# Performance work log

Hardware: AMD Instinct MI355X
Metric: run time of the kernel (lower is better)

Reference implementation:

```python
import jax, jax.numpy as jnp
import numpy as np

HIDDEN = 4096
N_HEADS = 32
N_KV = 8
HEAD_DIM = HIDDEN // N_HEADS  # 128
ROT_DIM = int(HEAD_DIM * 0.5)  # partial_rotary_factor = 0.5 -> 64
ROPE_BASE = 1_000_000.0
EPS = 1e-6
T = 2048


def setup_inputs() -> dict:
    key = jax.random.key(0)
    k1, k2, k3, k4, k5 = jax.random.split(key, 5)
    qkv_out = (N_HEADS + 2 * N_KV) * HEAD_DIM  # 6144
    hidden_states = jax.random.normal(k1, (T, HIDDEN), dtype=jnp.float32)
    positions = jnp.arange(T, dtype=jnp.int32)
    w_qkv = jax.random.normal(k2, (HIDDEN, qkv_out), dtype=jnp.float32) * (HIDDEN ** -0.5)
    w_o = jax.random.normal(k3, (N_HEADS * HEAD_DIM, HIDDEN), dtype=jnp.float32) * ((N_HEADS * HEAD_DIM) ** -0.5)
    q_norm_w = jnp.ones((HEAD_DIM,), dtype=jnp.float32) + 0.01 * jax.random.normal(k4, (HEAD_DIM,), dtype=jnp.float32)
    k_norm_w = jnp.ones((HEAD_DIM,), dtype=jnp.float32) + 0.01 * jax.random.normal(k5, (HEAD_DIM,), dtype=jnp.float32)
    return {"hidden_states": hidden_states, "positions": positions,
            "w_qkv": w_qkv, "w_o": w_o, "q_norm_w": q_norm_w, "k_norm_w": k_norm_w}


def _rms_norm(x, w):
    # x: [T, H, D]; normalize over last dim
    var = jnp.mean(jnp.square(x), axis=-1, keepdims=True)
    return x * jax.lax.rsqrt(var + EPS) * w


def _apply_rope(x, positions):
    # neox-style rotary on first ROT_DIM dims of head_dim; rest passes through
    half = ROT_DIM // 2
    inv_freq = 1.0 / (ROPE_BASE ** (jnp.arange(0, ROT_DIM, 2, dtype=jnp.float32) / ROT_DIM))
    freqs = positions.astype(jnp.float32)[:, None] * inv_freq[None, :]  # [T, half]
    cos = jnp.cos(freqs)[:, None, :]  # [T, 1, half]
    sin = jnp.sin(freqs)[:, None, :]
    x_rot, x_pass = x[..., :ROT_DIM], x[..., ROT_DIM:]
    x1, x2 = x_rot[..., :half], x_rot[..., half:]
    rot = jnp.concatenate([x1 * cos - x2 * sin, x2 * cos + x1 * sin], axis=-1)
    return jnp.concatenate([rot, x_pass], axis=-1)


def reference(hidden_states, positions, w_qkv, w_o, q_norm_w, k_norm_w):
    q_size = N_HEADS * HEAD_DIM
    kv_size = N_KV * HEAD_DIM
    qkv = hidden_states @ w_qkv  # [T, q+2kv]
    q = qkv[:, :q_size].reshape(-1, N_HEADS, HEAD_DIM)
    k = qkv[:, q_size:q_size + kv_size].reshape(-1, N_KV, HEAD_DIM)
    v = qkv[:, q_size + kv_size:].reshape(-1, N_KV, HEAD_DIM)
    q = _rms_norm(q, q_norm_w)
    k = _rms_norm(k, k_norm_w)
    q = _apply_rope(q, positions)
    k = _apply_rope(k, positions)
    # GQA: repeat kv heads
    rep = N_HEADS // N_KV
    k = jnp.repeat(k, rep, axis=1)  # [T, H, D]
    v = jnp.repeat(v, rep, axis=1)
    scale = HEAD_DIM ** -0.5
    scores = jnp.einsum('thd,shd->hts', q, k) * scale  # [H, T, T]
    t = hidden_states.shape[0]
    causal = jnp.tril(jnp.ones((t, t), dtype=bool))
    scores = jnp.where(causal[None], scores, jnp.float32(-1e30))
    probs = jax.nn.softmax(scores, axis=-1)
    o = jnp.einsum('hts,shd->thd', probs, v).reshape(t, N_HEADS * HEAD_DIM)
    return o @ w_o
```

## Files before the change

kernel.cpp:

```cpp
#include <hip/hip_runtime.h>
#include <math.h>

#define HIDDEN 4096
#define QKV_N 6144
#define T_LEN 2048
#define HD 128
#define N_HEADS 32
#define N_KV 8
#define SCALE 0.08838834764831845f

typedef unsigned short u16;
typedef unsigned int u32;
typedef __attribute__((ext_vector_type(8))) short bf16x8;
typedef __attribute__((ext_vector_type(4))) float f32x4;

__device__ __forceinline__ u16 f2b(float x) {
  u32 u = __builtin_bit_cast(u32, x);
  u += 0x7fffu + ((u >> 16) & 1u);
  return (u16)(u >> 16);
}

typedef const __attribute__((address_space(1))) void* gas_ptr;
typedef __attribute__((address_space(3))) void* las_ptr;
__device__ __forceinline__ void gll16(const void* g, void* l) {
  __builtin_amdgcn_global_load_lds((gas_ptr)g, (las_ptr)l, 16, 0, 0);
}

__global__ __launch_bounds__(256) void cast_bf16_kernel(
    const float* __restrict__ in, u16* __restrict__ out) {
  const size_t i = ((size_t)blockIdx.x * 256 + threadIdx.x) * 4;
  f32x4 v = *(const f32x4*)(in + i);
  ushort4 o;
  o.x = f2b(v[0]); o.y = f2b(v[1]); o.z = f2b(v[2]); o.w = f2b(v[3]);
  *(ushort4*)(out + i) = o;
}

__global__ __launch_bounds__(256) void transpose_cast_kernel(
    const float* __restrict__ W, u16* __restrict__ WT, int K, int N) {
  __shared__ float t[32][33];
  const int n0 = blockIdx.x * 32, k0 = blockIdx.y * 32;
  const int c = threadIdx.x & 31;
  const int r0 = threadIdx.x >> 5;
#pragma unroll
  for (int j = 0; j < 4; ++j) {
    const int r = r0 + 8 * j;
    t[c][r] = W[(size_t)(k0 + r) * N + n0 + c];
  }
  __syncthreads();
#pragma unroll
  for (int j = 0; j < 4; ++j) {
    const int n = r0 + 8 * j;
    WT[(size_t)(n0 + n) * K + k0 + c] = f2b(t[n][c]);
  }
}

template <int BM, int BN>
__global__ __launch_bounds__(512, 2) void gemm256_kernel(
    const u16* __restrict__ A, const u16* __restrict__ BT,
    float* __restrict__ C, int M, int N, int K) {
  constexpr int WCOLS = BN / 4;
  constexpr int NF = WCOLS / 16;
  constexpr int NF2 = NF / 2;
  constexpr int MF = BM / 32;
  constexpr int ALOADS = BM / 128;
  constexpr int BLOADS = BN / 128;
  constexpr int VMN = ALOADS + BLOADS;
  __shared__ __align__(16) u16 As[2][2][BM * 32];
  __shared__ __align__(16) u16 Bs[2][2][BN * 32];

  const int tid = threadIdx.x;
  const int w = tid >> 6, l = tid & 63;
  const int wr = w >> 2, wc = w & 3;
  const int m = l & 15, g = l >> 4;
  const int bm = blockIdx.y * BM, bn = blockIdx.x * BN;
  const int NT = K >> 6;

  size_t gA[2]; int sA[2];
  size_t gB[2]; int sB[2];
#pragma unroll
  for (int i = 0; i < ALOADS; ++i) {
    const int s = i * 512 + tid;
    const int r = s >> 2, o = s & 3;
    sA[i] = s * 8;
    gA[i] = (size_t)(bm + r) * K + (o ^ ((r >> 1) & 3)) * 8;
  }
#pragma unroll
  for (int i = 0; i < BLOADS; ++i) {
    const int s = i * 512 + tid;
    const int r = s >> 2, o = s & 3;
    sB[i] = s * 8;
    gB[i] = (size_t)(bn + r) * K + (o ^ ((r >> 1) & 3)) * 8;
  }

  const int foff = m * 32 + ((g ^ ((m >> 1) & 3)) * 8);
  const int abase = wr * (BM / 2) * 32;
  const int bbase = wc * WCOLS * 32;

#define STAGE_A(tile, kh)                                                      \
  {                                                                            \
    const size_t kofs = (size_t)(tile) * 64 + (kh) * 32;                       \
    u16* dst = &As[(tile) & 1][kh][0];                                         \
    gll16(A + gA[0] + kofs, dst + sA[0]);                                      \
    if constexpr (ALOADS > 1) gll16(A + gA[1] + kofs, dst + sA[1]);            \
  }
#define STAGE_B(tile, kh)                                                      \
  {                                                                            \
    const size_t kofs = (size_t)(tile) * 64 + (kh) * 32;                       \
    u16* dst = &Bs[(tile) & 1][kh][0];                                         \
    gll16(BT + gB[0] + kofs, dst + sB[0]);                                     \
    if constexpr (BLOADS > 1) gll16(BT + gB[1] + kofs, dst + sB[1]);           \
  }
#define VM_COUNTED()                                                           \
  {                                                                            \
    if constexpr (VMN == 4)                                                    \
      asm volatile("s_waitcnt vmcnt(4)" ::: "memory");                         \
    else                                                                       \
      asm volatile("s_waitcnt vmcnt(3)" ::: "memory");                         \
  }
#define PHASE(j, b, DO_STAGE, tn, VM)                                          \
  {                                                                            \
    constexpr int qn = (j) & 1, kh = (j) >> 1;                                 \
    if constexpr (qn == 0) {                                                   \
      _Pragma("unroll") for (int fm = 0; fm < MF; ++fm)                        \
          af[fm] = *(const bf16x8*)(&As[b][kh][abase + fm * 512 + foff]);      \
    }                                                                          \
    bf16x8 bf[NF2];                                                            \
    _Pragma("unroll") for (int fn = 0; fn < NF2; ++fn)                         \
        bf[fn] =                                                               \
        *(const bf16x8*)(&Bs[b][kh][bbase + (qn * NF2 + fn) * 512 + foff]);    \
    if constexpr (DO_STAGE) {                                                  \
      if constexpr ((j) == 0) STAGE_A(tn, 0);                                  \
      if constexpr ((j) == 1) STAGE_B(tn, 0);                                  \
      if constexpr ((j) == 2) STAGE_A(tn, 1);                                  \
      if constexpr ((j) == 3) STAGE_B(tn, 1);                                  \
    }                                                                          \
    asm volatile("" ::: "memory");                                             \
    __builtin_amdgcn_s_barrier();                                              \
    asm volatile("" ::: "memory");                                             \
    __builtin_amdgcn_s_setprio(1);                                             \
    _Pragma("unroll") for (int fm = 0; fm < MF; ++fm)                          \
        _Pragma("unroll") for (int fn = 0; fn < NF2; ++fn)                     \
        acc[fm][qn * NF2 + fn] = __builtin_amdgcn_mfma_f32_16x16x32_bf16(      \
            af[fm], bf[fn], acc[fm][qn * NF2 + fn], 0, 0, 0);                  \
    __builtin_amdgcn_s_setprio(0);                                             \
    asm volatile("" ::: "memory");                                             \
    if constexpr (((j) & 1) && (VM) == 0)                                      \
      asm volatile("s_waitcnt vmcnt(0)" ::: "memory");                         \
    if constexpr (((j) & 1) && (VM) == 1) VM_COUNTED();                        \
    __builtin_amdgcn_s_barrier();                                              \
    asm volatile("" ::: "memory");                                             \
  }

  f32x4 acc[MF][NF];
#pragma unroll
  for (int i = 0; i < MF; ++i)
#pragma unroll
    for (int j = 0; j < NF; ++j) acc[i][j] = (f32x4){0.f, 0.f, 0.f, 0.f};

  STAGE_A(0, 0); STAGE_B(0, 0); STAGE_A(0, 1); STAGE_B(0, 1);
  VM_COUNTED();
  __builtin_amdgcn_s_barrier();
  asm volatile("" ::: "memory");

  bf16x8 af[MF];
  for (int t = 0; t < NT - 1; ++t) {
    const int b = t & 1, tn = t + 1;
    PHASE(0, b, true, tn, 1);
    PHASE(1, b, true, tn, 1);
    PHASE(2, b, true, tn, 1);
    PHASE(3, b, true, tn, 1);
  }
  {
    const int b = (NT - 1) & 1;
    PHASE(0, b, false, 0, 2);
    PHASE(1, b, false, 0, 0);
    PHASE(2, b, false, 0, 2);
    PHASE(3, b, false, 0, 2);
  }
#undef PHASE
#undef VM_COUNTED
#undef STAGE_B
#undef STAGE_A

#pragma unroll
  for (int fm = 0; fm < MF; ++fm) {
    const int row = bm + wr * (BM / 2) + fm * 16 + g * 4;
#pragma unroll
    for (int fn = 0; fn < NF; ++fn) {
      const int col = bn + wc * WCOLS + fn * 16 + m;
      float* cp = C + (size_t)row * N + col;
#pragma unroll
      for (int r = 0; r < 4; ++r) cp[(size_t)r * N] = acc[fm][fn][r];
    }
  }
}

__global__ __launch_bounds__(128) void normrope_pack_kernel(
    const float* __restrict__ qkv, const int* __restrict__ positions,
    const float* __restrict__ qw, const float* __restrict__ kw,
    u16* __restrict__ Qp, u16* __restrict__ Kp) {
  const int t = blockIdx.x;
  const int hh = blockIdx.y;
  const int d = threadIdx.x;
  const bool isq = hh < N_HEADS;
  const int col = isq ? hh * HD : HIDDEN + (hh - N_HEADS) * HD;
  const float* row = qkv + (size_t)t * QKV_N + col;
  const float* w = isq ? qw : kw;

  float x = row[d];
  float ss = x * x;
#pragma unroll
  for (int off = 32; off >= 1; off >>= 1) ss += __shfl_xor(ss, off);
  __shared__ float wsum[2];
  __shared__ float xs[128];
  if ((d & 63) == 0) wsum[d >> 6] = ss;
  __syncthreads();
  const float tot = wsum[0] + wsum[1];
  const float inv = rsqrtf(tot * (1.f / 128.f) + 1e-6f);
  const float xn = x * inv * w[d];
  xs[d] = xn;
  __syncthreads();

  float outv;
  if (d < 64) {
    const int idx = d & 31;
    const float invf = powf(1.0e6f, -(float)idx * (1.0f / 32.0f));
    const float fr = (float)positions[t] * invf;
    const float c = cosf(fr), s = sinf(fr);
    const float x1 = xs[idx], x2 = xs[idx + 32];
    outv = (d < 32) ? (x1 * c - x2 * s) : (x2 * c + x1 * s);
  } else {
    outv = xn;
  }
  if (isq) {
    Qp[((size_t)hh * T_LEN + t) * HD + d] = f2b(outv * SCALE);
  } else {
    Kp[((size_t)(hh - N_HEADS) * T_LEN + t) * HD + d] = f2b(outv);
  }
}

__global__ __launch_bounds__(256) void vtrans_kernel(
    const float* __restrict__ qkv, u16* __restrict__ Vtp) {
  __shared__ float tile[32][132];
  const int t0 = blockIdx.x * 32;
  const int kvh = blockIdx.y;
  const int tv = threadIdx.x >> 3;
  const int c0 = (threadIdx.x & 7) * 16;
  const float* src =
      qkv + (size_t)(t0 + tv) * QKV_N + (HIDDEN + 1024) + kvh * HD + c0;
#pragma unroll
  for (int u = 0; u < 4; ++u)
    *(f32x4*)&tile[tv][c0 + 4 * u] = *(const f32x4*)(src + 4 * u);
  __syncthreads();
  const int dd = threadIdx.x >> 1;
  const int half = threadIdx.x & 1;
  u16 buf[16];
#pragma unroll
  for (int p = 0; p < 16; ++p) buf[p] = f2b(tile[half * 16 + p][dd]);
  u16* dst = Vtp + ((size_t)kvh * HD + dd) * T_LEN + t0 + half * 16;
  *(uint4*)dst = *(uint4*)&buf[0];
  *(uint4*)(dst + 8) = *(uint4*)&buf[8];
}

__global__ __launch_bounds__(256, 3) void attn4_kernel(
    const u16* __restrict__ Qp, const u16* __restrict__ Kp,
    const u16* __restrict__ Vtp, u16* __restrict__ outB) {
  __shared__ __align__(16) u16 Qs[64 * 128];
  __shared__ __align__(16) u16 Ks[2 * 32 * 128];
  __shared__ __align__(16) u16 Vts[2 * 128 * 32];
  __shared__ __align__(16) u16 Plds[4 * 16 * 32];

  const int bx = blockIdx.x;
  const int h = blockIdx.y;
  const int kvh = h >> 2;
  const int tid = threadIdx.x;
  const int w = tid >> 6, l = tid & 63;
  const int g = l >> 4, m = l & 15;

  const u16* kbase = Kp + (size_t)kvh * T_LEN * HD;
  const u16* vbase = Vtp + (size_t)kvh * HD * T_LEN;
  u16* pl = Plds + w * 512;

#define STAGE_KV(jt, b)                                                        \
  {                                                                            \
    _Pragma("unroll") for (int p = 0; p < 2; ++p) {                            \
      const int krow = p * 16 + w * 4 + (l >> 4);                              \
      const int kg = (l & 15) ^ (krow & 7);                                    \
      gll16(kbase + (size_t)((jt) * 32 + krow) * 128 + kg * 8,                 \
            Ks + (b) * 4096 + p * 2048 + w * 512 + l * 8);                     \
      const int dv = p * 64 + w * 16 + (l >> 2);                               \
      const int vg = (l & 3) ^ ((dv >> 1) & 3);                                \
      gll16(vbase + (size_t)dv * T_LEN + (jt) * 32 + vg * 8,                   \
            Vts + (b) * 4096 + p * 2048 + w * 512 + l * 8);                    \
    }                                                                          \
  }

  for (int job = 0; job < 2; ++job) {
    const int qb = job ? bx : 31 - bx;
    const int t0 = qb * 64;
    const int NT = 2 * (qb + 1);

    {
      const u16* qbase = Qp + ((size_t)h * T_LEN + t0) * HD;
#pragma unroll
      for (int p = 0; p < 4; ++p) {
        const int row = p * 16 + w * 4 + (l >> 4);
        const int gr = (l & 15) ^ (row & 7);
        gll16(qbase + row * 128 + gr * 8, Qs + p * 2048 + w * 512 + l * 8);
      }
    }
    STAGE_KV(0, 0);
    __syncthreads();

    bf16x8 qf[4];
    {
      const u16* qr = Qs + (w * 16 + m) * 128;
#pragma unroll
      for (int kk = 0; kk < 4; ++kk)
        qf[kk] = *(const bf16x8*)(qr + (((kk * 4 + g) ^ (m & 7)) * 8));
    }

    f32x4 o[8];
#pragma unroll
    for (int n = 0; n < 8; ++n) o[n] = (f32x4){0.f, 0.f, 0.f, 0.f};
    float mrun = -1e30f, lrun = 0.f;

    for (int jt = 0; jt < NT; ++jt) {
      const int b = jt & 1;
      if (jt + 1 < NT) STAGE_KV(jt + 1, b ^ 1);

      f32x4 s[2];
      s[0] = (f32x4){0.f, 0.f, 0.f, 0.f};
      s[1] = (f32x4){0.f, 0.f, 0.f, 0.f};
      __builtin_amdgcn_s_setprio(1);
#pragma unroll
      for (int f = 0; f < 2; ++f) {
        const u16* kr = Ks + b * 4096 + (f * 16 + m) * 128;
#pragma unroll
        for (int kk = 0; kk < 4; ++kk) {
          bf16x8 kf = *(const bf16x8*)(kr + (((kk * 4 + g) ^ (m & 7)) * 8));
          s[f] =
              __builtin_amdgcn_mfma_f32_16x16x32_bf16(kf, qf[kk], s[f], 0, 0, 0);
        }
      }
      __builtin_amdgcn_s_setprio(0);

      if (jt >= NT - 2) {
        const int qg = t0 + w * 16 + m;
        const int kvb = jt * 32 + g * 4;
#pragma unroll
        for (int f = 0; f < 2; ++f)
#pragma unroll
          for (int r = 0; r < 4; ++r)
            if (kvb + f * 16 + r > qg) s[f][r] = -1e30f;
      }

      float pm = fmaxf(fmaxf(fmaxf(s[0][0], s[0][1]), fmaxf(s[0][2], s[0][3])),
                       fmaxf(fmaxf(s[1][0], s[1][1]), fmaxf(s[1][2], s[1][3])));
      pm = fmaxf(pm, __shfl_xor(pm, 16));
      pm = fmaxf(pm, __shfl_xor(pm, 32));
      if (!__all(pm <= mrun + 8.f)) {
        const float mn = fmaxf(mrun, pm);
        const float sc = __expf(mrun - mn);
        mrun = mn;
        lrun *= sc;
        f32x4 scr;
#pragma unroll
        for (int r = 0; r < 4; ++r) scr[r] = __shfl(sc, g * 4 + r);
#pragma unroll
        for (int n = 0; n < 8; ++n) o[n] *= scr;
      }
      float ps = 0.f;
#pragma unroll
      for (int f = 0; f < 2; ++f)
#pragma unroll
        for (int r = 0; r < 4; ++r) {
          s[f][r] = __expf(s[f][r] - mrun);
          ps += s[f][r];
        }
      ps += __shfl_xor(ps, 16);
      ps += __shfl_xor(ps, 32);
      lrun += ps;

      {
        const u32 a0 = (u32)f2b(s[0][0]) | ((u32)f2b(s[0][1]) << 16);
        const u32 a1 = (u32)f2b(s[0][2]) | ((u32)f2b(s[0][3]) << 16);
        const u32 b0 = (u32)f2b(s[1][0]) | ((u32)f2b(s[1][1]) << 16);
        const u32 b1 = (u32)f2b(s[1][2]) | ((u32)f2b(s[1][3]) << 16);
        *(uint2*)(pl + m * 32 + ((g ^ (m >> 1)) * 4)) = make_uint2(a0, a1);
        *(uint2*)(pl + m * 32 + (((g + 4) ^ (m >> 1)) * 4)) = make_uint2(b0, b1);
      }

      bf16x8 pa;
      {
        const uint2 lo =
            *(const uint2*)(pl + m * 32 + (((2 * g) ^ (m >> 1)) * 4));
        const uint2 hi =
            *(const uint2*)(pl + m * 32 + (((2 * g + 1) ^ (m >> 1)) * 4));
        union { u32 u[4]; bf16x8 v; } pu;
        pu.u[0] = lo.x; pu.u[1] = lo.y; pu.u[2] = hi.x; pu.u[3] = hi.y;
        pa = pu.v;
      }

      __builtin_amdgcn_s_setprio(1);
#pragma unroll
      for (int n = 0; n < 8; ++n) {
        const int dd = n * 16 + m;
        bf16x8 vf = *(const bf16x8*)(Vts + b * 4096 + dd * 32 +
                                     ((g ^ ((dd >> 1) & 3)) * 8));
        o[n] = __builtin_amdgcn_mfma_f32_16x16x32_bf16(pa, vf, o[n], 0, 0, 0);
      }
      __builtin_amdgcn_s_setprio(0);
      __syncthreads();
    }

    float li[4];
#pragma unroll
    for (int r = 0; r < 4; ++r) li[r] = 1.f / __shfl(lrun, g * 4 + r);
    u16* ob = outB + (size_t)(t0 + w * 16 + g * 4) * HIDDEN + h * HD + m;
#pragma unroll
    for (int n = 0; n < 8; ++n)
#pragma unroll
      for (int r = 0; r < 4; ++r)
        ob[(size_t)r * HIDDEN + n * 16] = f2b(o[n][r] * li[r]);
  }
#undef STAGE_KV
}

extern "C" void kernel_launch(void* const* d_in, const int* in_sizes, int n_in,
                              void* d_out, int out_size, void* d_ws,
                              size_t ws_size, hipStream_t stream) {
  const float* hidden = (const float*)d_in[0];
  const int* positions = (const int*)d_in[1];
  const float* w_qkv = (const float*)d_in[2];
  const float* w_o = (const float*)d_in[3];
  const float* q_norm_w = (const float*)d_in[4];
  const float* k_norm_w = (const float*)d_in[5];
  float* out = (float*)d_out;

  u16* hiddenB = (u16*)d_ws;
  u16* Qp = hiddenB;
  u16* wqkvT = hiddenB + (size_t)T_LEN * HIDDEN;
  u16* woT = wqkvT + (size_t)QKV_N * HIDDEN;
  float* qkv = (float*)(woT + (size_t)HIDDEN * HIDDEN);
  u16* attnB = (u16*)(qkv + (size_t)T_LEN * QKV_N);
  u16* Kp = attnB + (size_t)T_LEN * HIDDEN;
  u16* Vtp = Kp + (size_t)N_KV * T_LEN * HD;

  cast_bf16_kernel<<<(T_LEN * HIDDEN) / 1024, 256, 0, stream>>>(hidden, hiddenB);
  transpose_cast_kernel<<<dim3(QKV_N / 32, HIDDEN / 32), 256, 0, stream>>>(
      w_qkv, wqkvT, HIDDEN, QKV_N);
  transpose_cast_kernel<<<dim3(HIDDEN / 32, HIDDEN / 32), 256, 0, stream>>>(
      w_o, woT, HIDDEN, HIDDEN);

  gemm256_kernel<256, 256><<<dim3(QKV_N / 256, T_LEN / 256), 512, 0, stream>>>(
      hiddenB, wqkvT, qkv, T_LEN, QKV_N, HIDDEN);
  normrope_pack_kernel<<<dim3(T_LEN, N_HEADS + N_KV), 128, 0, stream>>>(
      qkv, positions, q_norm_w, k_norm_w, Qp, Kp);
  vtrans_kernel<<<dim3(T_LEN / 32, N_KV), 256, 0, stream>>>(qkv, Vtp);
  attn4_kernel<<<dim3(16, N_HEADS), 256, 0, stream>>>(Qp, Kp, Vtp, attnB);
  gemm256_kernel<128, 256><<<dim3(HIDDEN / 256, T_LEN / 128), 512, 0, stream>>>(
      attnB, woT, out, T_LEN, HIDDEN, HIDDEN);
}
```

Baseline: 368.2 us.

## Double attention query tile per block to reuse K/V across two row groups

Each attention block now processes 128 query rows instead of 64, split into two 64-row halves per wave, so every staged K/V tile and its K fragments feed two sets of MFMAs. The causal early half skips work when a KV tile lies past its rows. This halves K/V global and LDS traffic per query row. In exchange, register pressure and LDS use rise, occupancy drops from 3 to 2 blocks per CU, and the grid shrinks to 256 blocks, which may underfill the GPU.

Result: slower. 394.1 us (+7.1%).

```diff
diff --git a/kernel.cpp b/kernel.cpp
--- a/kernel.cpp
+++ b/kernel.cpp
@@ -262,13 +262,13 @@
   *(uint4*)(dst + 8) = *(uint4*)&buf[8];
 }
 
-__global__ __launch_bounds__(256, 3) void attn4_kernel(
+__global__ __launch_bounds__(256, 2) void attn5_kernel(
     const u16* __restrict__ Qp, const u16* __restrict__ Kp,
     const u16* __restrict__ Vtp, u16* __restrict__ outB) {
-  __shared__ __align__(16) u16 Qs[64 * 128];
+  __shared__ __align__(16) u16 Qs[128 * 128];
   __shared__ __align__(16) u16 Ks[2 * 32 * 128];
   __shared__ __align__(16) u16 Vts[2 * 128 * 32];
-  __shared__ __align__(16) u16 Plds[4 * 16 * 32];
+  __shared__ __align__(16) u16 Plds[2 * 4 * 16 * 32];
 
   const int bx = blockIdx.x;
   const int h = blockIdx.y;
@@ -279,7 +279,8 @@
 
   const u16* kbase = Kp + (size_t)kvh * T_LEN * HD;
   const u16* vbase = Vtp + (size_t)kvh * HD * T_LEN;
-  u16* pl = Plds + w * 512;
+  u16* pl0 = Plds + w * 512;
+  u16* pl1 = Plds + 2048 + w * 512;
 
 #define STAGE_KV(jt, b)                                                        \
   {                                                                            \
@@ -294,16 +295,57 @@
             Vts + (b) * 4096 + p * 2048 + w * 512 + l * 8);                    \
     }                                                                          \
   }
+#define P_BOUNCE(sv, pl, pa)                                                   \
+  {                                                                            \
+    const u32 a0 = (u32)f2b(sv[0][0]) | ((u32)f2b(sv[0][1]) << 16);            \
+    const u32 a1 = (u32)f2b(sv[0][2]) | ((u32)f2b(sv[0][3]) << 16);            \
+    const u32 b0 = (u32)f2b(sv[1][0]) | ((u32)f2b(sv[1][1]) << 16);            \
+    const u32 b1 = (u32)f2b(sv[1][2]) | ((u32)f2b(sv[1][3]) << 16);            \
+    *(uint2*)((pl) + m * 32 + ((g ^ (m >> 1)) * 4)) = make_uint2(a0, a1);      \
+    *(uint2*)((pl) + m * 32 + (((g + 4) ^ (m >> 1)) * 4)) = make_uint2(b0, b1);\
+    const uint2 lo = *(const uint2*)((pl) + m * 32 + (((2 * g) ^ (m >> 1)) * 4)); \
+    const uint2 hi =                                                           \
+        *(const uint2*)((pl) + m * 32 + (((2 * g + 1) ^ (m >> 1)) * 4));       \
+    union { u32 u[4]; bf16x8 v; } pu;                                          \
+    pu.u[0] = lo.x; pu.u[1] = lo.y; pu.u[2] = hi.x; pu.u[3] = hi.y;            \
+    pa = pu.v;                                                                 \
+  }
+#define SOFTMAX_SET(sv, mrun, lrun, ov)                                        \
+  {                                                                            \
+    float pm = fmaxf(fmaxf(fmaxf(sv[0][0], sv[0][1]), fmaxf(sv[0][2], sv[0][3])), \
+                     fmaxf(fmaxf(sv[1][0], sv[1][1]), fmaxf(sv[1][2], sv[1][3]))); \
+    pm = fmaxf(pm, __shfl_xor(pm, 16));                                        \
+    pm = fmaxf(pm, __shfl_xor(pm, 32));                                        \
+    if (!__all(pm <= mrun + 8.f)) {                                            \
+      const float mn = fmaxf(mrun, pm);                                        \
+      const float sc = __expf(mrun - mn);                                      \
+      mrun = mn;                                                               \
+      lrun *= sc;                                                              \
+      f32x4 scr;                                                               \
+      _Pragma("unroll") for (int r = 0; r < 4; ++r) scr[r] =                   \
+          __shfl(sc, g * 4 + r);                                               \
+      _Pragma("unroll") for (int n = 0; n < 8; ++n) ov[n] *= scr;              \
+    }                                                                          \
+    float ps = 0.f;                                                            \
+    _Pragma("unroll") for (int f = 0; f < 2; ++f)                              \
+        _Pragma("unroll") for (int r = 0; r < 4; ++r) {                        \
+      sv[f][r] = __expf(sv[f][r] - mrun);                                      \
+      ps += sv[f][r];                                                          \
+    }                                                                          \
+    ps += __shfl_xor(ps, 16);                                                  \
+    ps += __shfl_xor(ps, 32);                                                  \
+    lrun += ps;                                                                \
+  }
 
   for (int job = 0; job < 2; ++job) {
-    const int qb = job ? bx : 31 - bx;
-    const int t0 = qb * 64;
-    const int NT = 2 * (qb + 1);
+    const int qb = job ? bx : 15 - bx;
+    const int t0 = qb * 128;
+    const int NT = 4 * (qb + 1);
 
     {
       const u16* qbase = Qp + ((size_t)h * T_LEN + t0) * HD;
 #pragma unroll
-      for (int p = 0; p < 4; ++p) {
+      for (int p = 0; p < 8; ++p) {
         const int row = p * 16 + w * 4 + (l >> 4);
         const int gr = (l & 15) ^ (row & 7);
         gll16(qbase + row * 128 + gr * 8, Qs + p * 2048 + w * 512 + l * 8);
@@ -312,94 +354,87 @@
     STAGE_KV(0, 0);
     __syncthreads();
 
-    bf16x8 qf[4];
+    bf16x8 qf0[4], qf1[4];
     {
-      const u16* qr = Qs + (w * 16 + m) * 128;
-#pragma unroll
-      for (int kk = 0; kk < 4; ++kk)
-        qf[kk] = *(const bf16x8*)(qr + (((kk * 4 + g) ^ (m & 7)) * 8));
+      const u16* qr0 = Qs + (w * 16 + m) * 128;
+      const u16* qr1 = Qs + (64 + w * 16 + m) * 128;
+#pragma unroll
+      for (int kk = 0; kk < 4; ++kk) {
+        const int go = ((kk * 4 + g) ^ (m & 7)) * 8;
+        qf0[kk] = *(const bf16x8*)(qr0 + go);
+        qf1[kk] = *(const bf16x8*)(qr1 + go);
+      }
     }
 
-    f32x4 o[8];
-#pragma unroll
-    for (int n = 0; n < 8; ++n) o[n] = (f32x4){0.f, 0.f, 0.f, 0.f};
-    float mrun = -1e30f, lrun = 0.f;
+    f32x4 o0[8], o1[8];
+#pragma unroll
+    for (int n = 0; n < 8; ++n) {
+      o0[n] = (f32x4){0.f, 0.f, 0.f, 0.f};
+      o1[n] = (f32x4){0.f, 0.f, 0.f, 0.f};
+    }
+    float mrun0 = -1e30f, lrun0 = 0.f, mrun1 = -1e30f, lrun1 = 0.f;
+    const int qg0 = t0 + w * 16 + m;
+    const int qg1 = t0 + 64 + w * 16 + m;
 
     for (int jt = 0; jt < NT; ++jt) {
       const int b = jt & 1;
       if (jt + 1 < NT) STAGE_KV(jt + 1, b ^ 1);
-
-      f32x4 s[2];
-      s[0] = (f32x4){0.f, 0.f, 0.f, 0.f};
-      s[1] = (f32x4){0.f, 0.f, 0.f, 0.f};
+      const bool do0 = (jt * 32 <= t0 + 63);
+
+      bf16x8 kfr[8];
+#pragma unroll
+      for (int f = 0; f < 2; ++f)
+#pragma unroll
+        for (int kk = 0; kk < 4; ++kk)
+          kfr[f * 4 + kk] = *(const bf16x8*)(
+              Ks + b * 4096 + (f * 16 + m) * 128 + (((kk * 4 + g) ^ (m & 7)) * 8));
+
+      f32x4 s1[2];
+      s1[0] = (f32x4){0.f, 0.f, 0.f, 0.f};
+      s1[1] = (f32x4){0.f, 0.f, 0.f, 0.f};
+      f32x4 s0[2];
       __builtin_amdgcn_s_setprio(1);
 #pragma unroll
-      for (int f = 0; f < 2; ++f) {
-        const u16* kr = Ks + b * 4096 + (f * 16 + m) * 128;
-#pragma unroll
-        for (int kk = 0; kk < 4; ++kk) {
-          bf16x8 kf = *(const bf16x8*)(kr + (((kk * 4 + g) ^ (m & 7)) * 8));
-          s[f] =
-              __builtin_amdgcn_mfma_f32_16x16x32_bf16(kf, qf[kk], s[f], 0, 0, 0);
-        }
+      for (int f = 0; f < 2; ++f)
+#pragma unroll
+        for (int kk = 0; kk < 4; ++kk)
+          s1[f] = __builtin_amdgcn_mfma_f32_16x16x32_bf16(kfr[f * 4 + kk],
+                                                          qf1[kk], s1[f], 0, 0, 0);
+      if (do0) {
+        s0[0] = (f32x4){0.f, 0.f, 0.f, 0.f};
+        s0[1] = (f32x4){0.f, 0.f, 0.f, 0.f};
+#pragma unroll
+        for (int f = 0; f < 2; ++f)
+#pragma unroll
+          for (int kk = 0; kk < 4; ++kk)
+            s0[f] = __builtin_amdgcn_mfma_f32_16x16x32_bf16(
+                kfr[f * 4 + kk], qf0[kk], s0[f], 0, 0, 0);
       }
       __builtin_amdgcn_s_setprio(0);
 
       if (jt >= NT - 2) {
-        const int qg = t0 + w * 16 + m;
         const int kvb = jt * 32 + g * 4;
 #pragma unroll
         for (int f = 0; f < 2; ++f)
 #pragma unroll
           for (int r = 0; r < 4; ++r)
-            if (kvb + f * 16 + r > qg) s[f][r] = -1e30f;
-      }
-
-      float pm = fmaxf(fmaxf(fmaxf(s[0][0], s[0][1]), fmaxf(s[0][2], s[0][3])),
-                       fmaxf(fmaxf(s[1][0], s[1][1]), fmaxf(s[1][2], s[1][3])));
-      pm = fmaxf(pm, __shfl_xor(pm, 16));
-      pm = fmaxf(pm, __shfl_xor(pm, 32));
-      if (!__all(pm <= mrun + 8.f)) {
-        const float mn = fmaxf(mrun, pm);
-        const float sc = __expf(mrun - mn);
-        mrun = mn;
-        lrun *= sc;
-        f32x4 scr;
-#pragma unroll
-        for (int r = 0; r < 4; ++r) scr[r] = __shfl(sc, g * 4 + r);
-#pragma unroll
-        for (int n = 0; n < 8; ++n) o[n] *= scr;
-      }
-      float ps = 0.f;
-#pragma unroll
-      for (int f = 0; f < 2; ++f)
-#pragma unroll
-        for (int r = 0; r < 4; ++r) {
-          s[f][r] = __expf(s[f][r] - mrun);
-          ps += s[f][r];
-        }
-      ps += __shfl_xor(ps, 16);
-      ps += __shfl_xor(ps, 32);
-      lrun += ps;
-
-      {
-        const u32 a0 = (u32)f2b(s[0][0]) | ((u32)f2b(s[0][1]) << 16);
-        const u32 a1 = (u32)f2b(s[0][2]) | ((u32)f2b(s[0][3]) << 16);
-        const u32 b0 = (u32)f2b(s[1][0]) | ((u32)f2b(s[1][1]) << 16);
-        const u32 b1 = (u32)f2b(s[1][2]) | ((u32)f2b(s[1][3]) << 16);
-        *(uint2*)(pl + m * 32 + ((g ^ (m >> 1)) * 4)) = make_uint2(a0, a1);
-        *(uint2*)(pl + m * 32 + (((g + 4) ^ (m >> 1)) * 4)) = make_uint2(b0, b1);
-      }
-
-      bf16x8 pa;
-      {
-        const uint2 lo =
-            *(const uint2*)(pl + m * 32 + (((2 * g) ^ (m >> 1)) * 4));
-        const uint2 hi =
-            *(const uint2*)(pl + m * 32 + (((2 * g + 1) ^ (m >> 1)) * 4));
-        union { u32 u[4]; bf16x8 v; } pu;
-        pu.u[0] = lo.x; pu.u[1] = lo.y; pu.u[2] = hi.x; pu.u[3] = hi.y;
-        pa = pu.v;
+            if (kvb + f * 16 + r > qg1) s1[f][r] = -1e30f;
+      }
+      if (do0 && jt >= NT - 4) {
+        const int kvb = jt * 32 + g * 4;
+#pragma unroll
+        for (int f = 0; f < 2; ++f)
+#pragma unroll
+          for (int r = 0; r < 4; ++r)
+            if (kvb + f * 16 + r > qg0) s0[f][r] = -1e30f;
+      }
+
+      bf16x8 pa0, pa1;
+      SOFTMAX_SET(s1, mrun1, lrun1, o1);
+      P_BOUNCE(s1, pl1, pa1);
+      if (do0) {
+        SOFTMAX_SET(s0, mrun0, lrun0, o0);
+        P_BOUNCE(s0, pl0, pa0);
       }
 
       __builtin_amdgcn_s_setprio(1);
@@ -408,22 +443,32 @@
         const int dd = n * 16 + m;
         bf16x8 vf = *(const bf16x8*)(Vts + b * 4096 + dd * 32 +
                                      ((g ^ ((dd >> 1) & 3)) * 8));
-        o[n] = __builtin_amdgcn_mfma_f32_16x16x32_bf16(pa, vf, o[n], 0, 0, 0);
+        o1[n] = __builtin_amdgcn_mfma_f32_16x16x32_bf16(pa1, vf, o1[n], 0, 0, 0);
+        if (do0)
+          o0[n] = __builtin_amdgcn_mfma_f32_16x16x32_bf16(pa0, vf, o0[n], 0, 0, 0);
       }
       __builtin_amdgcn_s_setprio(0);
       __syncthreads();
     }
 
-    float li[4];
-#pragma unroll
-    for (int r = 0; r < 4; ++r) li[r] = 1.f / __shfl(lrun, g * 4 + r);
-    u16* ob = outB + (size_t)(t0 + w * 16 + g * 4) * HIDDEN + h * HD + m;
+    float li0[4], li1[4];
+#pragma unroll
+    for (int r = 0; r < 4; ++r) {
+      li0[r] = 1.f / __shfl(lrun0, g * 4 + r);
+      li1[r] = 1.f / __shfl(lrun1, g * 4 + r);
+    }
+    u16* ob0 = outB + (size_t)(t0 + w * 16 + g * 4) * HIDDEN + h * HD + m;
+    u16* ob1 = ob0 + (size_t)64 * HIDDEN;
 #pragma unroll
     for (int n = 0; n < 8; ++n)
 #pragma unroll
-      for (int r = 0; r < 4; ++r)
-        ob[(size_t)r * HIDDEN + n * 16] = f2b(o[n][r] * li[r]);
-  }
+      for (int r = 0; r < 4; ++r) {
+        ob0[(size_t)r * HIDDEN + n * 16] = f2b(o0[n][r] * li0[r]);
+        ob1[(size_t)r * HIDDEN + n * 16] = f2b(o1[n][r] * li1[r]);
+      }
+  }
+#undef SOFTMAX_SET
+#undef P_BOUNCE
 #undef STAGE_KV
 }
 
@@ -458,7 +503,7 @@
   normrope_pack_kernel<<<dim3(T_LEN, N_HEADS + N_KV), 128, 0, stream>>>(
       qkv, positions, q_norm_w, k_norm_w, Qp, Kp);
   vtrans_kernel<<<dim3(T_LEN / 32, N_KV), 256, 0, stream>>>(qkv, Vtp);
-  attn4_kernel<<<dim3(16, N_HEADS), 256, 0, stream>>>(Qp, Kp, Vtp, attnB);
+  attn5_kernel<<<dim3(8, N_HEADS), 256, 0, stream>>>(Qp, Kp, Vtp, attnB);
   gemm256_kernel<128, 256><<<dim3(HIDDEN / 256, T_LEN / 128), 512, 0, stream>>>(
       attnB, woT, out, T_LEN, HIDDEN, HIDDEN);
 }
```
